# Performance work log

Hardware: AMD Instinct MI355X
Metric: run time of the kernel (lower is better)

The kernel has to match this reference:

```python
import math
import jax, jax.numpy as jnp
import numpy as np

N_FEAT = 4096
EPS = 1e-05
SQRT_LUT = jnp.array([math.isqrt(i * 256 + 128) for i in range(256)], dtype=jnp.int32)


def _ste_round(x):
    # straight-through round: forward round, backward identity
    return x + jax.lax.stop_gradient(jnp.round(x) - x)


def _sqrt_rounded(d):
    # vectorized integer LUT sqrt of d (int32, values in [0, 65535])
    bits = jnp.arange(16, dtype=jnp.int32)
    msb = jnp.sum((d[..., None] >> bits) > 0, axis=-1).astype(jnp.int32) - 1  # bit_length - 1
    k = msb // 2
    norm_shift = (7 - k) * 2
    d_norm = d << norm_shift
    lut_addr = (d_norm >> 8) & 255
    mant = SQRT_LUT[lut_addr]
    q_floor = mant >> (7 - k)
    boundary = q_floor * q_floor + q_floor
    res = jnp.where(d > boundary, q_floor + 1, q_floor)
    return jnp.where(d == 0, 0, res)


def setup_inputs() -> dict:
    key = jax.random.key(0)
    kx, = jax.random.split(key, 1)
    x = jax.random.normal(kx, (8192, N_FEAT), dtype=jnp.float32)
    gamma = jnp.ones((N_FEAT,), dtype=jnp.float32)
    beta = jnp.zeros((N_FEAT,), dtype=jnp.float32)
    return {"x": x, "gamma": gamma, "beta": beta}


def reference(x, gamma, beta):
    # input quantization (per-tensor symmetric int8)
    scale_in = jnp.maximum(jnp.max(jnp.abs(x)) / 127.0, 1e-08)
    x_int = jnp.clip(_ste_round(x / scale_in), -127.0, 127.0)
    x_q = x_int * scale_in
    Ex = jnp.sum(x_q, axis=1, keepdims=True)  # [B,1]
    # LUT-based squaring: split |x_int| into high/low nibbles, x^2 = H^2*256 + 2*H*L*16 + L^2
    X_abs = jnp.abs(x_int).astype(jnp.int32)  # int cast detaches (matches .long())
    H = X_abs >> 4
    L = X_abs & 15
    x_squared_int = (H * H * 256 + H * L * 32 + L * L).astype(jnp.float32)
    x_squared_q = x_squared_int * scale_in ** 2
    Ex2 = jnp.sum(x_squared_q, axis=1, keepdims=True)  # [B,1]
    mu = Ex / N_FEAT
    var = jnp.maximum(Ex2 / N_FEAT - mu * mu, 0.0)
    var_int = jnp.clip(jnp.round(var), 1.0, 2.0 ** 16 - 1).astype(jnp.int32)
    std_int = _sqrt_rounded(var_int).astype(jnp.float32)  # [B,1]
    inv_std = 1.0 / jnp.maximum(std_int, EPS)
    x_norm = (x_q - mu) * inv_std
    y = x_norm * gamma + beta
    # output re-quantization
    scale_out = jnp.maximum(jnp.max(jnp.abs(y)) / 127.0, 1e-08)
    y_int = jnp.clip(_ste_round(y / scale_out), -127.0, 127.0)
    return y_int * scale_out
```

## Files before the change

### kernel.cpp

```cpp
#include <hip/hip_runtime.h>
#include <stdint.h>

#define NFEAT 4096
#define UI_PER_ROW (NFEAT / 4)

#define NSLOT 64
#define SLOT_STRIDE 16

__device__ __forceinline__ int isqrt_floor_small(int v) {
    int m = (int)sqrtf((float)v);
    m -= (m * m > v);
    m += ((m + 1) * (m + 1) <= v);
    return m;
}

__device__ __forceinline__ int sqrt_rounded_ref(int d) {
    if (d <= 0) return 0;
    int msb = 31 - __clz(d);
    int k = msb >> 1;
    int sh = (7 - k) * 2;
    int dn = d << sh;
    int la = (dn >> 8) & 255;
    int mant = isqrt_floor_small(la * 256 + 128);
    int qf = mant >> (7 - k);
    int bnd = qf * qf + qf;
    return (d > bnd) ? (qf + 1) : qf;
}

__device__ __forceinline__ float div_rn(float x, float s, float rs) {
    float q0 = x * rs;
    float r  = fmaf(-s, q0, x);
    return fmaf(r, rs, q0);
}

__device__ __forceinline__ float slot_max(const unsigned* __restrict__ slots) {
    unsigned v = slots[(threadIdx.x & 63) * SLOT_STRIDE];
#pragma unroll
    for (int off = 32; off; off >>= 1) {
        unsigned o = (unsigned)__shfl_xor((int)v, off);
        v = v > o ? v : o;
    }
    return __uint_as_float(v);
}

__global__ __launch_bounds__(256, 4) void absmax_kernel(const float* __restrict__ x,
                                                        int n4,
                                                        unsigned* __restrict__ hx) {
    const float4* x4 = (const float4*)x;
    int i = blockIdx.x * 256 + threadIdx.x;
    const int stride = gridDim.x * 256;
    float m = 0.0f;
    for (; i + 3 * stride < n4; i += 4 * stride) {
        float4 a = x4[i];
        float4 b = x4[i + stride];
        float4 c = x4[i + 2 * stride];
        float4 d = x4[i + 3 * stride];
        float ma = fmaxf(fmaxf(fabsf(a.x), fabsf(a.y)), fmaxf(fabsf(a.z), fabsf(a.w)));
        float mb = fmaxf(fmaxf(fabsf(b.x), fabsf(b.y)), fmaxf(fabsf(b.z), fabsf(b.w)));
        float mc = fmaxf(fmaxf(fabsf(c.x), fabsf(c.y)), fmaxf(fabsf(c.z), fabsf(c.w)));
        float md = fmaxf(fmaxf(fabsf(d.x), fabsf(d.y)), fmaxf(fabsf(d.z), fabsf(d.w)));
        m = fmaxf(m, fmaxf(fmaxf(ma, mb), fmaxf(mc, md)));
    }
    for (; i < n4; i += stride) {
        float4 a = x4[i];
        m = fmaxf(m, fmaxf(fmaxf(fabsf(a.x), fabsf(a.y)), fmaxf(fabsf(a.z), fabsf(a.w))));
    }
#pragma unroll
    for (int off = 32; off; off >>= 1) m = fmaxf(m, __shfl_down(m, off));
    __shared__ float smax[4];
    int lane = threadIdx.x & 63, w = threadIdx.x >> 6;
    if (lane == 0) smax[w] = m;
    __syncthreads();
    if (threadIdx.x == 0) {
        m = fmaxf(fmaxf(smax[0], smax[1]), fmaxf(smax[2], smax[3]));
        atomicMax(hx + (blockIdx.x & (NSLOT - 1)) * SLOT_STRIDE, __float_as_uint(m));
    }
}

template <bool WQ>
__global__ __launch_bounds__(256, 4) void rowstat_kernel(
    const float* __restrict__ x, const float* __restrict__ gamma,
    const float* __restrict__ beta, const unsigned* __restrict__ hx,
    unsigned* __restrict__ hy,
    float* __restrict__ row_mu, float* __restrict__ row_inv,
    uint32_t* __restrict__ xq8) {
#pragma clang fp contract(off)
    const int row = blockIdx.x;
    const int t = threadIdx.x;
    const float4* xr = (const float4*)(x + (size_t)row * NFEAT);
    float4 v0 = xr[t];
    float4 v1 = xr[256 + t];
    float4 v2 = xr[512 + t];
    float4 v3 = xr[768 + t];
    const float s  = fmaxf(slot_max(hx) / 127.0f, 1e-8f);
    const float rs = 1.0f / s;

    float xv[16] = {v0.x, v0.y, v0.z, v0.w, v1.x, v1.y, v1.z, v1.w,
                    v2.x, v2.y, v2.z, v2.w, v3.x, v3.y, v3.z, v3.w};
    int xi[16];
    int s1 = 0, s2 = 0;
#pragma unroll
    for (int k = 0; k < 16; ++k) {
        float q = rintf(div_rn(xv[k], s, rs));
        q = fminf(fmaxf(q, -127.0f), 127.0f);
        int qi = (int)q;
        xi[k] = qi;
        s1 += qi;
        s2 += qi * qi;
    }
    if (WQ) {
        uint32_t* xw = xq8 + (size_t)row * UI_PER_ROW;
#pragma unroll
        for (int g = 0; g < 4; ++g) {
            uint32_t p = (uint32_t)(xi[4 * g + 0] & 255) |
                         ((uint32_t)(xi[4 * g + 1] & 255) << 8) |
                         ((uint32_t)(xi[4 * g + 2] & 255) << 16) |
                         ((uint32_t)xi[4 * g + 3] << 24);
            xw[g * 256 + t] = p;
        }
    }
#pragma unroll
    for (int off = 32; off; off >>= 1) {
        s1 += __shfl_down(s1, off);
        s2 += __shfl_down(s2, off);
    }
    __shared__ int a1[4], a2[4];
    __shared__ float smu, sinv;
    const int lane = t & 63, w = t >> 6;
    if (lane == 0) { a1[w] = s1; a2[w] = s2; }
    __syncthreads();
    if (t == 0) {
        int Exi = a1[0] + a1[1] + a1[2] + a1[3];
        int Ex2i = a2[0] + a2[1] + a2[2] + a2[3];
        float Ex = (float)Exi * s;
        float Ex2 = (float)Ex2i * s * s;
        float mu = Ex / (float)NFEAT;
        float var = fmaxf(Ex2 / (float)NFEAT - mu * mu, 0.0f);
        float vr = fminf(fmaxf(rintf(var), 1.0f), 65535.0f);
        int std_int = sqrt_rounded_ref((int)vr);
        float inv_std = 1.0f / fmaxf((float)std_int, 1e-5f);
        row_mu[row] = mu;
        row_inv[row] = inv_std;
        smu = mu;
        sinv = inv_std;
    }
    __syncthreads();
    const float mu = smu, inv = sinv;
    float ym = 0.0f;
#pragma unroll
    for (int g = 0; g < 4; ++g) {
        float4 gm = ((const float4*)gamma)[g * 256 + t];
        float4 bt = ((const float4*)beta)[g * 256 + t];
        float gv[4] = {gm.x, gm.y, gm.z, gm.w};
        float bv[4] = {bt.x, bt.y, bt.z, bt.w};
#pragma unroll
        for (int j = 0; j < 4; ++j) {
            float xq = (float)xi[g * 4 + j] * s;
            float xn = (xq - mu) * inv;
            float y = xn * gv[j] + bv[j];
            ym = fmaxf(ym, fabsf(y));
        }
    }
#pragma unroll
    for (int off = 32; off; off >>= 1) ym = fmaxf(ym, __shfl_down(ym, off));
    __shared__ float aym[4];
    if (lane == 0) aym[w] = ym;
    __syncthreads();
    if (t == 0) {
        float m = fmaxf(fmaxf(aym[0], aym[1]), fmaxf(aym[2], aym[3]));
        atomicMax(hy + (row & (NSLOT - 1)) * SLOT_STRIDE, __float_as_uint(m));
    }
}

__global__ __launch_bounds__(256, 4) void quantout_q_kernel(
    const uint32_t* __restrict__ xq8, const float* __restrict__ gamma,
    const float* __restrict__ beta, const unsigned* __restrict__ hx,
    const unsigned* __restrict__ hy,
    const float* __restrict__ row_mu, const float* __restrict__ row_inv,
    float* __restrict__ out) {
#pragma clang fp contract(off)
    const int row = blockIdx.x;
    const int t = threadIdx.x;
    const uint32_t* xr = xq8 + (size_t)row * UI_PER_ROW;
    uint32_t p0 = xr[t];
    uint32_t p1 = xr[256 + t];
    uint32_t p2 = xr[512 + t];
    uint32_t p3 = xr[768 + t];
    const float s_in  = fmaxf(slot_max(hx) / 127.0f, 1e-8f);
    const float s_out = fmaxf(slot_max(hy) / 127.0f, 1e-8f);
    const float rso = 1.0f / s_out;
    const float mu = row_mu[row], inv = row_inv[row];
    uint32_t pp[4] = {p0, p1, p2, p3};
    float4* outr = (float4*)(out + (size_t)row * NFEAT);
#pragma unroll
    for (int g = 0; g < 4; ++g) {
        uint32_t p = pp[g];
        float4 gm = ((const float4*)gamma)[g * 256 + t];
        float4 bt = ((const float4*)beta)[g * 256 + t];
        float gv[4] = {gm.x, gm.y, gm.z, gm.w};
        float bv[4] = {bt.x, bt.y, bt.z, bt.w};
        int xs[4] = {(int)(int8_t)(p & 255), (int)(int8_t)((p >> 8) & 255),
                     (int)(int8_t)((p >> 16) & 255), (int)(int8_t)((p >> 24) & 255)};
        float o[4];
#pragma unroll
        for (int j = 0; j < 4; ++j) {
            float xq = (float)xs[j] * s_in;
            float xn = (xq - mu) * inv;
            float y = xn * gv[j] + bv[j];
            float q = rintf(div_rn(y, s_out, rso));
            q = fminf(fmaxf(q, -127.0f), 127.0f);
            o[j] = q * s_out;
        }
        outr[g * 256 + t] = make_float4(o[0], o[1], o[2], o[3]);
    }
}

__global__ __launch_bounds__(256, 4) void quantout_f_kernel(
    const float* __restrict__ x, const float* __restrict__ gamma,
    const float* __restrict__ beta, const unsigned* __restrict__ hx,
    const unsigned* __restrict__ hy,
    const float* __restrict__ row_mu, const float* __restrict__ row_inv,
    float* __restrict__ out) {
#pragma clang fp contract(off)
    const int row = blockIdx.x;
    const int t = threadIdx.x;
    const float4* xr = (const float4*)(x + (size_t)row * NFEAT);
    float4 w0 = xr[t];
    float4 w1 = xr[256 + t];
    float4 w2 = xr[512 + t];
    float4 w3 = xr[768 + t];
    const float s_in  = fmaxf(slot_max(hx) / 127.0f, 1e-8f);
    const float s_out = fmaxf(slot_max(hy) / 127.0f, 1e-8f);
    const float rsi = 1.0f / s_in;
    const float rso = 1.0f / s_out;
    const float mu = row_mu[row], inv = row_inv[row];
    float4 vv[4] = {w0, w1, w2, w3};
    float4* outr = (float4*)(out + (size_t)row * NFEAT);
#pragma unroll
    for (int g = 0; g < 4; ++g) {
        float4 v = vv[g];
        float4 gm = ((const float4*)gamma)[g * 256 + t];
        float4 bt = ((const float4*)beta)[g * 256 + t];
        float xv[4] = {v.x, v.y, v.z, v.w};
        float gv[4] = {gm.x, gm.y, gm.z, gm.w};
        float bv[4] = {bt.x, bt.y, bt.z, bt.w};
        float o[4];
#pragma unroll
        for (int j = 0; j < 4; ++j) {
            float q = rintf(div_rn(xv[j], s_in, rsi));
            q = fminf(fmaxf(q, -127.0f), 127.0f);
            float xq = q * s_in;
            float xn = (xq - mu) * inv;
            float y = xn * gv[j] + bv[j];
            float qq = rintf(div_rn(y, s_out, rso));
            qq = fminf(fmaxf(qq, -127.0f), 127.0f);
            o[j] = qq * s_out;
        }
        outr[g * 256 + t] = make_float4(o[0], o[1], o[2], o[3]);
    }
}

extern "C" void kernel_launch(void* const* d_in, const int* in_sizes, int n_in,
                              void* d_out, int out_size, void* d_ws, size_t ws_size,
                              hipStream_t stream) {
    const float* x = (const float*)d_in[0];
    const float* gamma = (const float*)d_in[1];
    const float* beta = (const float*)d_in[2];
    float* out = (float*)d_out;

    const int total = in_sizes[0];
    const int rows = total / NFEAT;

    char* ws = (char*)d_ws;
    unsigned* hx = (unsigned*)ws;
    unsigned* hy = (unsigned*)(ws + 4096);
    float* row_mu = (float*)(ws + 8192);
    float* row_inv = row_mu + rows;
    size_t xq_off = (8192 + (size_t)rows * 8 + 255) & ~(size_t)255;
    uint32_t* xq8 = (uint32_t*)(ws + xq_off);
    const bool use_q = ws_size >= xq_off + (size_t)total + 256;

    hipMemsetAsync(ws, 0, 8192, stream);

    absmax_kernel<<<2048, 256, 0, stream>>>(x, total / 4, hx);

    if (use_q) {
        rowstat_kernel<true><<<rows, 256, 0, stream>>>(x, gamma, beta, hx, hy,
                                                       row_mu, row_inv, xq8);
        quantout_q_kernel<<<rows, 256, 0, stream>>>(xq8, gamma, beta, hx, hy,
                                                    row_mu, row_inv, out);
    } else {
        rowstat_kernel<false><<<rows, 256, 0, stream>>>(x, gamma, beta, hx, hy,
                                                        row_mu, row_inv, nullptr);
        quantout_f_kernel<<<rows, 256, 0, stream>>>(x, gamma, beta, hx, hy,
                                                    row_mu, row_inv, out);
    }
}
```

Measured before the change: 275.3 us.

## Fuse absmax, row stats and requantization into one cooperative grid-synced kernel

Replaces the memset plus three separate launches with a single cooperative kernel of 256 blocks of 1024 threads. Each block owns 32 rows and uses grid-wide syncs between the global absmax, the row-statistics/output-absmax pass and the final requantization pass. Per-block partial maxima go to plain slots instead of atomics, and the int8 staging buffer is dropped, so x is re-read from global memory in the last pass. This removes launch gaps and the memset, but adds grid-sync cost, relies on cooperative launch co-residency, and reads x three times (128 MB each), which may partly hit in cache.

```diff
diff --git a/kernel.cpp b/kernel.cpp
--- a/kernel.cpp
+++ b/kernel.cpp
@@ -1,8 +1,14 @@
 #include <hip/hip_runtime.h>
+#include <hip/hip_cooperative_groups.h>
 #include <stdint.h>
+
+namespace cg = cooperative_groups;
 
 #define NFEAT 4096
 #define UI_PER_ROW (NFEAT / 4)
+#define GRID 256
+#define BLK 1024
+#define ROWS_PB 32
 
 #define NSLOT 64
 #define SLOT_STRIDE 16
@@ -33,7 +39,182 @@
     return fmaf(r, rs, q0);
 }
 
-__device__ __forceinline__ float slot_max(const unsigned* __restrict__ slots) {
+__device__ __forceinline__ float slots256_max(const unsigned* __restrict__ s, int lane) {
+    unsigned v = s[lane];
+    unsigned a = s[lane + 64], b = s[lane + 128], c = s[lane + 192];
+    v = v > a ? v : a;
+    v = v > b ? v : b;
+    v = v > c ? v : c;
+#pragma unroll
+    for (int off = 32; off; off >>= 1) {
+        unsigned o = (unsigned)__shfl_xor((int)v, off);
+        v = v > o ? v : o;
+    }
+    return __uint_as_float(v);
+}
+
+__global__ __launch_bounds__(BLK, 4) void fused_kernel(
+    const float* __restrict__ x, const float* __restrict__ gamma,
+    const float* __restrict__ beta, float* __restrict__ out,
+    unsigned* __restrict__ slot, unsigned* __restrict__ slot2, int rows) {
+#pragma clang fp contract(off)
+    cg::grid_group gridg = cg::this_grid();
+    const int bid = blockIdx.x;
+    const int t = threadIdx.x;
+    const int lane = t & 63;
+    const int wave = t >> 6;
+
+    __shared__ int a1s[16], a2s[16];
+    __shared__ float redf[16];
+    __shared__ float smu[ROWS_PB], sinv[ROWS_PB];
+
+    {
+        const float4* x4 = (const float4*)x;
+        const int n4 = rows * (NFEAT / 4);
+        const int stride = GRID * BLK;
+        int i = bid * BLK + t;
+        float m = 0.0f;
+        for (; i + 3 * stride < n4; i += 4 * stride) {
+            float4 a = x4[i];
+            float4 b = x4[i + stride];
+            float4 c = x4[i + 2 * stride];
+            float4 d = x4[i + 3 * stride];
+            float ma = fmaxf(fmaxf(fabsf(a.x), fabsf(a.y)), fmaxf(fabsf(a.z), fabsf(a.w)));
+            float mb = fmaxf(fmaxf(fabsf(b.x), fabsf(b.y)), fmaxf(fabsf(b.z), fabsf(b.w)));
+            float mc = fmaxf(fmaxf(fabsf(c.x), fabsf(c.y)), fmaxf(fabsf(c.z), fabsf(c.w)));
+            float md = fmaxf(fmaxf(fabsf(d.x), fabsf(d.y)), fmaxf(fabsf(d.z), fabsf(d.w)));
+            m = fmaxf(m, fmaxf(fmaxf(ma, mb), fmaxf(mc, md)));
+        }
+        for (; i < n4; i += stride) {
+            float4 a = x4[i];
+            m = fmaxf(m, fmaxf(fmaxf(fabsf(a.x), fabsf(a.y)), fmaxf(fabsf(a.z), fabsf(a.w))));
+        }
+#pragma unroll
+        for (int off = 32; off; off >>= 1) m = fmaxf(m, __shfl_down(m, off));
+        if (lane == 0) redf[wave] = m;
+        __syncthreads();
+        if (t == 0) {
+            float mm = redf[0];
+#pragma unroll
+            for (int i2 = 1; i2 < 16; ++i2) mm = fmaxf(mm, redf[i2]);
+            slot[bid] = __float_as_uint(mm);
+        }
+    }
+    gridg.sync();
+
+    const float s  = fmaxf(slots256_max(slot, lane) / 127.0f, 1e-8f);
+    const float rs = 1.0f / s;
+    const int rb = t >> 8;
+    const int tr = t & 255;
+    const int nb = ROWS_PB / 4;
+    float ym = 0.0f;
+    for (int b = 0; b < nb; ++b) {
+        const int r = bid * ROWS_PB + b * 4 + rb;
+        const float4* xr = (const float4*)(x + (size_t)r * NFEAT);
+        float4 v0 = xr[tr];
+        float4 v1 = xr[256 + tr];
+        float4 v2 = xr[512 + tr];
+        float4 v3 = xr[768 + tr];
+        float xv[16] = {v0.x, v0.y, v0.z, v0.w, v1.x, v1.y, v1.z, v1.w,
+                        v2.x, v2.y, v2.z, v2.w, v3.x, v3.y, v3.z, v3.w};
+        int xi[16];
+        int s1 = 0, s2 = 0;
+#pragma unroll
+        for (int k = 0; k < 16; ++k) {
+            float q = rintf(div_rn(xv[k], s, rs));
+            q = fminf(fmaxf(q, -127.0f), 127.0f);
+            int qi = (int)q;
+            xi[k] = qi;
+            s1 += qi;
+            s2 += qi * qi;
+        }
+#pragma unroll
+        for (int off = 32; off; off >>= 1) {
+            s1 += __shfl_down(s1, off);
+            s2 += __shfl_down(s2, off);
+        }
+        if (lane == 0) { a1s[wave] = s1; a2s[wave] = s2; }
+        __syncthreads();
+        if (tr == 0) {
+            const int w0 = rb * 4;
+            int Exi  = a1s[w0] + a1s[w0 + 1] + a1s[w0 + 2] + a1s[w0 + 3];
+            int Ex2i = a2s[w0] + a2s[w0 + 1] + a2s[w0 + 2] + a2s[w0 + 3];
+            float Ex  = (float)Exi * s;
+            float Ex2 = (float)Ex2i * s * s;
+            float mu  = Ex / (float)NFEAT;
+            float var = fmaxf(Ex2 / (float)NFEAT - mu * mu, 0.0f);
+            float vr  = fminf(fmaxf(rintf(var), 1.0f), 65535.0f);
+            int std_int = sqrt_rounded_ref((int)vr);
+            float inv = 1.0f / fmaxf((float)std_int, 1e-5f);
+            smu[b * 4 + rb]  = mu;
+            sinv[b * 4 + rb] = inv;
+        }
+        __syncthreads();
+        const float mu = smu[b * 4 + rb], inv = sinv[b * 4 + rb];
+#pragma unroll
+        for (int g = 0; g < 4; ++g) {
+            float4 gm = ((const float4*)gamma)[g * 256 + tr];
+            float4 bt = ((const float4*)beta)[g * 256 + tr];
+            float gv[4] = {gm.x, gm.y, gm.z, gm.w};
+            float bv[4] = {bt.x, bt.y, bt.z, bt.w};
+#pragma unroll
+            for (int j = 0; j < 4; ++j) {
+                float xq = (float)xi[g * 4 + j] * s;
+                float xn = (xq - mu) * inv;
+                float y = xn * gv[j] + bv[j];
+                ym = fmaxf(ym, fabsf(y));
+            }
+        }
+    }
+#pragma unroll
+    for (int off = 32; off; off >>= 1) ym = fmaxf(ym, __shfl_down(ym, off));
+    if (lane == 0) redf[wave] = ym;
+    __syncthreads();
+    if (t == 0) {
+        float mm = redf[0];
+#pragma unroll
+        for (int i2 = 1; i2 < 16; ++i2) mm = fmaxf(mm, redf[i2]);
+        slot2[bid] = __float_as_uint(mm);
+    }
+    gridg.sync();
+
+    const float so  = fmaxf(slots256_max(slot2, lane) / 127.0f, 1e-8f);
+    const float rso = 1.0f / so;
+    for (int b = 0; b < nb; ++b) {
+        const int r = bid * ROWS_PB + b * 4 + rb;
+        const float4* xr = (const float4*)(x + (size_t)r * NFEAT);
+        float4 v0 = xr[tr];
+        float4 v1 = xr[256 + tr];
+        float4 v2 = xr[512 + tr];
+        float4 v3 = xr[768 + tr];
+        float xv[16] = {v0.x, v0.y, v0.z, v0.w, v1.x, v1.y, v1.z, v1.w,
+                        v2.x, v2.y, v2.z, v2.w, v3.x, v3.y, v3.z, v3.w};
+        const float mu = smu[b * 4 + rb], inv = sinv[b * 4 + rb];
+        float4* outr = (float4*)(out + (size_t)r * NFEAT);
+#pragma unroll
+        for (int g = 0; g < 4; ++g) {
+            float4 gm = ((const float4*)gamma)[g * 256 + tr];
+            float4 bt = ((const float4*)beta)[g * 256 + tr];
+            float gv[4] = {gm.x, gm.y, gm.z, gm.w};
+            float bv[4] = {bt.x, bt.y, bt.z, bt.w};
+            float o[4];
+#pragma unroll
+            for (int j = 0; j < 4; ++j) {
+                float q = rintf(div_rn(xv[g * 4 + j], s, rs));
+                q = fminf(fmaxf(q, -127.0f), 127.0f);
+                float xq = q * s;
+                float xn = (xq - mu) * inv;
+                float y = xn * gv[j] + bv[j];
+                float qq = rintf(div_rn(y, so, rso));
+                qq = fminf(fmaxf(qq, -127.0f), 127.0f);
+                o[j] = qq * so;
+            }
+            outr[g * 256 + tr] = make_float4(o[0], o[1], o[2], o[3]);
+        }
+    }
+}
+
+__device__ __forceinline__ float slot_max64(const unsigned* __restrict__ slots) {
     unsigned v = slots[(threadIdx.x & 63) * SLOT_STRIDE];
 #pragma unroll
     for (int off = 32; off; off >>= 1) {
@@ -77,13 +258,11 @@
     }
 }
 
-template <bool WQ>
 __global__ __launch_bounds__(256, 4) void rowstat_kernel(
     const float* __restrict__ x, const float* __restrict__ gamma,
     const float* __restrict__ beta, const unsigned* __restrict__ hx,
     unsigned* __restrict__ hy,
-    float* __restrict__ row_mu, float* __restrict__ row_inv,
-    uint32_t* __restrict__ xq8) {
+    float* __restrict__ row_mu, float* __restrict__ row_inv) {
 #pragma clang fp contract(off)
     const int row = blockIdx.x;
     const int t = threadIdx.x;
@@ -92,7 +271,7 @@
     float4 v1 = xr[256 + t];
     float4 v2 = xr[512 + t];
     float4 v3 = xr[768 + t];
-    const float s  = fmaxf(slot_max(hx) / 127.0f, 1e-8f);
+    const float s  = fmaxf(slot_max64(hx) / 127.0f, 1e-8f);
     const float rs = 1.0f / s;
 
     float xv[16] = {v0.x, v0.y, v0.z, v0.w, v1.x, v1.y, v1.z, v1.w,
@@ -108,24 +287,13 @@
         s1 += qi;
         s2 += qi * qi;
     }
-    if (WQ) {
-        uint32_t* xw = xq8 + (size_t)row * UI_PER_ROW;
-#pragma unroll
-        for (int g = 0; g < 4; ++g) {
-            uint32_t p = (uint32_t)(xi[4 * g + 0] & 255) |
-                         ((uint32_t)(xi[4 * g + 1] & 255) << 8) |
-                         ((uint32_t)(xi[4 * g + 2] & 255) << 16) |
-                         ((uint32_t)xi[4 * g + 3] << 24);
-            xw[g * 256 + t] = p;
-        }
-    }
 #pragma unroll
     for (int off = 32; off; off >>= 1) {
         s1 += __shfl_down(s1, off);
         s2 += __shfl_down(s2, off);
     }
     __shared__ int a1[4], a2[4];
-    __shared__ float smu, sinv;
+    __shared__ float smu1, sinv1;
     const int lane = t & 63, w = t >> 6;
     if (lane == 0) { a1[w] = s1; a2[w] = s2; }
     __syncthreads();
@@ -141,11 +309,11 @@
         float inv_std = 1.0f / fmaxf((float)std_int, 1e-5f);
         row_mu[row] = mu;
         row_inv[row] = inv_std;
-        smu = mu;
-        sinv = inv_std;
+        smu1 = mu;
+        sinv1 = inv_std;
     }
     __syncthreads();
-    const float mu = smu, inv = sinv;
+    const float mu = smu1, inv = sinv1;
     float ym = 0.0f;
 #pragma unroll
     for (int g = 0; g < 4; ++g) {
@@ -169,49 +337,6 @@
     if (t == 0) {
         float m = fmaxf(fmaxf(aym[0], aym[1]), fmaxf(aym[2], aym[3]));
         atomicMax(hy + (row & (NSLOT - 1)) * SLOT_STRIDE, __float_as_uint(m));
-    }
-}
-
-__global__ __launch_bounds__(256, 4) void quantout_q_kernel(
-    const uint32_t* __restrict__ xq8, const float* __restrict__ gamma,
-    const float* __restrict__ beta, const unsigned* __restrict__ hx,
-    const unsigned* __restrict__ hy,
-    const float* __restrict__ row_mu, const float* __restrict__ row_inv,
-    float* __restrict__ out) {
-#pragma clang fp contract(off)
-    const int row = blockIdx.x;
-    const int t = threadIdx.x;
-    const uint32_t* xr = xq8 + (size_t)row * UI_PER_ROW;
-    uint32_t p0 = xr[t];
-    uint32_t p1 = xr[256 + t];
-    uint32_t p2 = xr[512 + t];
-    uint32_t p3 = xr[768 + t];
-    const float s_in  = fmaxf(slot_max(hx) / 127.0f, 1e-8f);
-    const float s_out = fmaxf(slot_max(hy) / 127.0f, 1e-8f);
-    const float rso = 1.0f / s_out;
-    const float mu = row_mu[row], inv = row_inv[row];
-    uint32_t pp[4] = {p0, p1, p2, p3};
-    float4* outr = (float4*)(out + (size_t)row * NFEAT);
-#pragma unroll
-    for (int g = 0; g < 4; ++g) {
-        uint32_t p = pp[g];
-        float4 gm = ((const float4*)gamma)[g * 256 + t];
-        float4 bt = ((const float4*)beta)[g * 256 + t];
-        float gv[4] = {gm.x, gm.y, gm.z, gm.w};
-        float bv[4] = {bt.x, bt.y, bt.z, bt.w};
-        int xs[4] = {(int)(int8_t)(p & 255), (int)(int8_t)((p >> 8) & 255),
-                     (int)(int8_t)((p >> 16) & 255), (int)(int8_t)((p >> 24) & 255)};
-        float o[4];
-#pragma unroll
-        for (int j = 0; j < 4; ++j) {
-            float xq = (float)xs[j] * s_in;
-            float xn = (xq - mu) * inv;
-            float y = xn * gv[j] + bv[j];
-            float q = rintf(div_rn(y, s_out, rso));
-            q = fminf(fmaxf(q, -127.0f), 127.0f);
-            o[j] = q * s_out;
-        }
-        outr[g * 256 + t] = make_float4(o[0], o[1], o[2], o[3]);
     }
 }
 
@@ -229,8 +354,8 @@
     float4 w1 = xr[256 + t];
     float4 w2 = xr[512 + t];
     float4 w3 = xr[768 + t];
-    const float s_in  = fmaxf(slot_max(hx) / 127.0f, 1e-8f);
-    const float s_out = fmaxf(slot_max(hy) / 127.0f, 1e-8f);
+    const float s_in  = fmaxf(slot_max64(hx) / 127.0f, 1e-8f);
+    const float s_out = fmaxf(slot_max64(hy) / 127.0f, 1e-8f);
     const float rsi = 1.0f / s_in;
     const float rso = 1.0f / s_out;
     const float mu = row_mu[row], inv = row_inv[row];
@@ -269,30 +394,30 @@
     float* out = (float*)d_out;
 
     const int total = in_sizes[0];
-    const int rows = total / NFEAT;
+    int rows = total / NFEAT;
 
     char* ws = (char*)d_ws;
+    unsigned* slot  = (unsigned*)ws;
+    unsigned* slot2 = (unsigned*)(ws + 2048);
+
+    if (rows == GRID * ROWS_PB) {
+        void* args[] = {(void*)&x, (void*)&gamma, (void*)&beta, (void*)&out,
+                        (void*)&slot, (void*)&slot2, (void*)&rows};
+        hipError_t e = hipLaunchCooperativeKernel((void*)fused_kernel,
+                                                  dim3(GRID), dim3(BLK),
+                                                  args, 0, stream);
+        if (e == hipSuccess) return;
+    }
+
     unsigned* hx = (unsigned*)ws;
     unsigned* hy = (unsigned*)(ws + 4096);
     float* row_mu = (float*)(ws + 8192);
     float* row_inv = row_mu + rows;
-    size_t xq_off = (8192 + (size_t)rows * 8 + 255) & ~(size_t)255;
-    uint32_t* xq8 = (uint32_t*)(ws + xq_off);
-    const bool use_q = ws_size >= xq_off + (size_t)total + 256;
 
     hipMemsetAsync(ws, 0, 8192, stream);
-
     absmax_kernel<<<2048, 256, 0, stream>>>(x, total / 4, hx);
-
-    if (use_q) {
-        rowstat_kernel<true><<<rows, 256, 0, stream>>>(x, gamma, beta, hx, hy,
-                                                       row_mu, row_inv, xq8);
-        quantout_q_kernel<<<rows, 256, 0, stream>>>(xq8, gamma, beta, hx, hy,
-                                                    row_mu, row_inv, out);
-    } else {
-        rowstat_kernel<false><<<rows, 256, 0, stream>>>(x, gamma, beta, hx, hy,
-                                                        row_mu, row_inv, nullptr);
-        quantout_f_kernel<<<rows, 256, 0, stream>>>(x, gamma, beta, hx, hy,
-                                                    row_mu, row_inv, out);
-    }
-}
+    rowstat_kernel<<<rows, 256, 0, stream>>>(x, gamma, beta, hx, hy,
+                                             row_mu, row_inv);
+    quantout_f_kernel<<<rows, 256, 0, stream>>>(x, gamma, beta, hx, hy,
+                                                row_mu, row_inv, out);
+}
```

After: 342.5 us. 1.24x slower.

## Replace atomic max slots with per-block partials and one-row-per-wave row stats

Applied to the files above, without the earlier changes.

The global absmax reductions now write one partial per block instead of doing atomicMax into 64 slots, which removes the memset launch and atomic contention. Consumers read and reduce up to 2048 partials per block in wave 0. Row statistics now run with one wave per row, using shuffle-only reductions and no block-level barrier for mu and variance. This adds redundant partial-reading work in every consumer block and may lower per-row memory parallelism.

```diff
diff --git a/kernel.cpp b/kernel.cpp
--- a/kernel.cpp
+++ b/kernel.cpp
@@ -2,10 +2,7 @@
 #include <stdint.h>
 
 #define NFEAT 4096
-#define UI_PER_ROW (NFEAT / 4)
-
-#define NSLOT 64
-#define SLOT_STRIDE 16
+#define ABS_GRID 2048
 
 __device__ __forceinline__ int isqrt_floor_small(int v) {
     int m = (int)sqrtf((float)v);
@@ -33,22 +30,27 @@
     return fmaf(r, rs, q0);
 }
 
-__device__ __forceinline__ float slot_max(const unsigned* __restrict__ slots) {
-    unsigned v = slots[(threadIdx.x & 63) * SLOT_STRIDE];
+__device__ __forceinline__ unsigned slots_max_u(const unsigned* __restrict__ s,
+                                                int n, int lane) {
+    unsigned v = 0;
+    for (int i = lane; i < n; i += 64) {
+        unsigned a = s[i];
+        v = v > a ? v : a;
+    }
 #pragma unroll
     for (int off = 32; off; off >>= 1) {
         unsigned o = (unsigned)__shfl_xor((int)v, off);
         v = v > o ? v : o;
     }
-    return __uint_as_float(v);
-}
-
-__global__ __launch_bounds__(256, 4) void absmax_kernel(const float* __restrict__ x,
-                                                        int n4,
-                                                        unsigned* __restrict__ hx) {
+    return v;
+}
+
+__global__ __launch_bounds__(256, 4) void absmax_ps(const float* __restrict__ x,
+                                                    int n4,
+                                                    unsigned* __restrict__ hx) {
     const float4* x4 = (const float4*)x;
     int i = blockIdx.x * 256 + threadIdx.x;
-    const int stride = gridDim.x * 256;
+    const int stride = ABS_GRID * 256;
     float m = 0.0f;
     for (; i + 3 * stride < n4; i += 4 * stride) {
         float4 a = x4[i];
@@ -73,28 +75,184 @@
     __syncthreads();
     if (threadIdx.x == 0) {
         m = fmaxf(fmaxf(smax[0], smax[1]), fmaxf(smax[2], smax[3]));
-        atomicMax(hx + (blockIdx.x & (NSLOT - 1)) * SLOT_STRIDE, __float_as_uint(m));
-    }
-}
-
-template <bool WQ>
-__global__ __launch_bounds__(256, 4) void rowstat_kernel(
+        hx[blockIdx.x] = __float_as_uint(m);
+    }
+}
+
+__global__ __launch_bounds__(256, 4) void rowstat_wave(
     const float* __restrict__ x, const float* __restrict__ gamma,
     const float* __restrict__ beta, const unsigned* __restrict__ hx,
     unsigned* __restrict__ hy,
     float* __restrict__ row_mu, float* __restrict__ row_inv,
     uint32_t* __restrict__ xq8) {
 #pragma clang fp contract(off)
+    const int bid = blockIdx.x;
+    const int t = threadIdx.x;
+    const int lane = t & 63;
+    const int wave = t >> 6;
+    const float4* g4 = (const float4*)gamma;
+    const float4* b4 = (const float4*)beta;
+
+    __shared__ float sS;
+    __shared__ float redf[4];
+
+    if (wave == 0) {
+        unsigned mb = slots_max_u(hx, ABS_GRID, lane);
+        if (lane == 0) sS = fmaxf(__uint_as_float(mb) / 127.0f, 1e-8f);
+    }
+    __syncthreads();
+    const float s  = sS;
+    const float rs = 1.0f / s;
+
+    const int row = bid * 4 + wave;
+    const float4* xr = (const float4*)(x + (size_t)row * NFEAT);
+
+    uint32_t pk[16];
+    int s1 = 0, s2 = 0;
+#pragma unroll 4
+    for (int c = 0; c < 16; ++c) {
+        float4 v = xr[c * 64 + lane];
+        float q0 = rintf(div_rn(v.x, s, rs));
+        float q1 = rintf(div_rn(v.y, s, rs));
+        float q2 = rintf(div_rn(v.z, s, rs));
+        float q3 = rintf(div_rn(v.w, s, rs));
+        q0 = fminf(fmaxf(q0, -127.0f), 127.0f);
+        q1 = fminf(fmaxf(q1, -127.0f), 127.0f);
+        q2 = fminf(fmaxf(q2, -127.0f), 127.0f);
+        q3 = fminf(fmaxf(q3, -127.0f), 127.0f);
+        int i0 = (int)q0, i1 = (int)q1, i2 = (int)q2, i3 = (int)q3;
+        pk[c] = (uint32_t)(i0 & 255) | ((uint32_t)(i1 & 255) << 8) |
+                ((uint32_t)(i2 & 255) << 16) | ((uint32_t)i3 << 24);
+        s1 += i0 + i1 + i2 + i3;
+        s2 += i0 * i0 + i1 * i1 + i2 * i2 + i3 * i3;
+    }
+#pragma unroll
+    for (int off = 32; off; off >>= 1) {
+        s1 += __shfl_xor(s1, off);
+        s2 += __shfl_xor(s2, off);
+    }
+    float Ex  = (float)s1 * s;
+    float Ex2 = (float)s2 * s * s;
+    float mu  = Ex / (float)NFEAT;
+    float var = fmaxf(Ex2 / (float)NFEAT - mu * mu, 0.0f);
+    float vr  = fminf(fmaxf(rintf(var), 1.0f), 65535.0f);
+    int sdi   = sqrt_rounded_ref((int)vr);
+    float inv = 1.0f / fmaxf((float)sdi, 1e-5f);
+    if (lane == 0) {
+        row_mu[row]  = mu;
+        row_inv[row] = inv;
+    }
+
+    uint32_t* xw = xq8 + (size_t)row * (NFEAT / 4);
+#pragma unroll 4
+    for (int c = 0; c < 16; ++c) xw[c * 64 + lane] = pk[c];
+
+    float ym = 0.0f;
+#pragma unroll 4
+    for (int c = 0; c < 16; ++c) {
+        uint32_t p = pk[c];
+        float4 gm = g4[c * 64 + lane];
+        float4 bt = b4[c * 64 + lane];
+        int i0 = (int)(int8_t)(p & 255);
+        int i1 = (int)(int8_t)((p >> 8) & 255);
+        int i2 = (int)(int8_t)((p >> 16) & 255);
+        int i3 = (int)(int8_t)((p >> 24) & 255);
+        float y0 = ((float)i0 * s - mu) * inv * gm.x + bt.x;
+        float y1 = ((float)i1 * s - mu) * inv * gm.y + bt.y;
+        float y2 = ((float)i2 * s - mu) * inv * gm.z + bt.z;
+        float y3 = ((float)i3 * s - mu) * inv * gm.w + bt.w;
+        ym = fmaxf(ym, fmaxf(fmaxf(fabsf(y0), fabsf(y1)),
+                             fmaxf(fabsf(y2), fabsf(y3))));
+    }
+#pragma unroll
+    for (int off = 32; off; off >>= 1) ym = fmaxf(ym, __shfl_down(ym, off));
+    if (lane == 0) redf[wave] = ym;
+    __syncthreads();
+    if (t == 0) {
+        hy[bid] = __float_as_uint(fmaxf(fmaxf(redf[0], redf[1]),
+                                        fmaxf(redf[2], redf[3])));
+    }
+}
+
+__global__ __launch_bounds__(256, 4) void quantout_q2(
+    const uint32_t* __restrict__ xq8, const float* __restrict__ gamma,
+    const float* __restrict__ beta, const unsigned* __restrict__ hx,
+    const unsigned* __restrict__ hy, int n_hy,
+    const float* __restrict__ row_mu, const float* __restrict__ row_inv,
+    float* __restrict__ out) {
+#pragma clang fp contract(off)
     const int row = blockIdx.x;
     const int t = threadIdx.x;
+    const int lane = t & 63;
+    const int wave = t >> 6;
+
+    __shared__ float sIn, sOut;
+    if (wave == 0) {
+        unsigned a = slots_max_u(hx, ABS_GRID, lane);
+        unsigned b = slots_max_u(hy, n_hy, lane);
+        if (lane == 0) {
+            sIn  = fmaxf(__uint_as_float(a) / 127.0f, 1e-8f);
+            sOut = fmaxf(__uint_as_float(b) / 127.0f, 1e-8f);
+        }
+    }
+    __syncthreads();
+    const float s_in  = sIn;
+    const float s_out = sOut;
+    const float rso = 1.0f / s_out;
+    const float mu = row_mu[row], inv = row_inv[row];
+
+    const uint32_t* xr = xq8 + (size_t)row * (NFEAT / 4);
+    uint32_t p0 = xr[t];
+    uint32_t p1 = xr[256 + t];
+    uint32_t p2 = xr[512 + t];
+    uint32_t p3 = xr[768 + t];
+    uint32_t pp[4] = {p0, p1, p2, p3};
+    float4* outr = (float4*)(out + (size_t)row * NFEAT);
+#pragma unroll
+    for (int g = 0; g < 4; ++g) {
+        uint32_t p = pp[g];
+        float4 gm = ((const float4*)gamma)[g * 256 + t];
+        float4 bt = ((const float4*)beta)[g * 256 + t];
+        float gv[4] = {gm.x, gm.y, gm.z, gm.w};
+        float bv[4] = {bt.x, bt.y, bt.z, bt.w};
+        int xs[4] = {(int)(int8_t)(p & 255), (int)(int8_t)((p >> 8) & 255),
+                     (int)(int8_t)((p >> 16) & 255), (int)(int8_t)((p >> 24) & 255)};
+        float o[4];
+#pragma unroll
+        for (int j = 0; j < 4; ++j) {
+            float xq = (float)xs[j] * s_in;
+            float xn = (xq - mu) * inv;
+            float y = xn * gv[j] + bv[j];
+            float q = rintf(div_rn(y, s_out, rso));
+            q = fminf(fmaxf(q, -127.0f), 127.0f);
+            o[j] = q * s_out;
+        }
+        outr[g * 256 + t] = make_float4(o[0], o[1], o[2], o[3]);
+    }
+}
+
+__global__ __launch_bounds__(256, 4) void rowstat_blk(
+    const float* __restrict__ x, const float* __restrict__ gamma,
+    const float* __restrict__ beta, const unsigned* __restrict__ hx,
+    unsigned* __restrict__ hy,
+    float* __restrict__ row_mu, float* __restrict__ row_inv) {
+#pragma clang fp contract(off)
+    const int row = blockIdx.x;
+    const int t = threadIdx.x;
+    const int lane = t & 63, w = t >> 6;
+    __shared__ float sS;
+    if (w == 0) {
+        unsigned mb = slots_max_u(hx, ABS_GRID, lane);
+        if (lane == 0) sS = fmaxf(__uint_as_float(mb) / 127.0f, 1e-8f);
+    }
+    __syncthreads();
+    const float s = sS;
+    const float rs = 1.0f / s;
     const float4* xr = (const float4*)(x + (size_t)row * NFEAT);
     float4 v0 = xr[t];
     float4 v1 = xr[256 + t];
     float4 v2 = xr[512 + t];
     float4 v3 = xr[768 + t];
-    const float s  = fmaxf(slot_max(hx) / 127.0f, 1e-8f);
-    const float rs = 1.0f / s;
-
     float xv[16] = {v0.x, v0.y, v0.z, v0.w, v1.x, v1.y, v1.z, v1.w,
                     v2.x, v2.y, v2.z, v2.w, v3.x, v3.y, v3.z, v3.w};
     int xi[16];
@@ -108,25 +266,13 @@
         s1 += qi;
         s2 += qi * qi;
     }
-    if (WQ) {
-        uint32_t* xw = xq8 + (size_t)row * UI_PER_ROW;
-#pragma unroll
-        for (int g = 0; g < 4; ++g) {
-            uint32_t p = (uint32_t)(xi[4 * g + 0] & 255) |
-                         ((uint32_t)(xi[4 * g + 1] & 255) << 8) |
-                         ((uint32_t)(xi[4 * g + 2] & 255) << 16) |
-                         ((uint32_t)xi[4 * g + 3] << 24);
-            xw[g * 256 + t] = p;
-        }
-    }
 #pragma unroll
     for (int off = 32; off; off >>= 1) {
         s1 += __shfl_down(s1, off);
         s2 += __shfl_down(s2, off);
     }
     __shared__ int a1[4], a2[4];
-    __shared__ float smu, sinv;
-    const int lane = t & 63, w = t >> 6;
+    __shared__ float smu1, sinv1;
     if (lane == 0) { a1[w] = s1; a2[w] = s2; }
     __syncthreads();
     if (t == 0) {
@@ -141,11 +287,11 @@
         float inv_std = 1.0f / fmaxf((float)std_int, 1e-5f);
         row_mu[row] = mu;
         row_inv[row] = inv_std;
-        smu = mu;
-        sinv = inv_std;
-    }
-    __syncthreads();
-    const float mu = smu, inv = sinv;
+        smu1 = mu;
+        sinv1 = inv_std;
+    }
+    __syncthreads();
+    const float mu = smu1, inv = sinv1;
     float ym = 0.0f;
 #pragma unroll
     for (int g = 0; g < 4; ++g) {
@@ -166,79 +312,40 @@
     __shared__ float aym[4];
     if (lane == 0) aym[w] = ym;
     __syncthreads();
-    if (t == 0) {
-        float m = fmaxf(fmaxf(aym[0], aym[1]), fmaxf(aym[2], aym[3]));
-        atomicMax(hy + (row & (NSLOT - 1)) * SLOT_STRIDE, __float_as_uint(m));
-    }
-}
-
-__global__ __launch_bounds__(256, 4) void quantout_q_kernel(
-    const uint32_t* __restrict__ xq8, const float* __restrict__ gamma,
+    if (t == 0)
+        hy[row] = __float_as_uint(fmaxf(fmaxf(aym[0], aym[1]),
+                                        fmaxf(aym[2], aym[3])));
+}
+
+__global__ __launch_bounds__(256, 4) void quantout_f2(
+    const float* __restrict__ x, const float* __restrict__ gamma,
     const float* __restrict__ beta, const unsigned* __restrict__ hx,
-    const unsigned* __restrict__ hy,
+    const unsigned* __restrict__ hy, int n_hy,
     const float* __restrict__ row_mu, const float* __restrict__ row_inv,
     float* __restrict__ out) {
 #pragma clang fp contract(off)
     const int row = blockIdx.x;
     const int t = threadIdx.x;
-    const uint32_t* xr = xq8 + (size_t)row * UI_PER_ROW;
-    uint32_t p0 = xr[t];
-    uint32_t p1 = xr[256 + t];
-    uint32_t p2 = xr[512 + t];
-    uint32_t p3 = xr[768 + t];
-    const float s_in  = fmaxf(slot_max(hx) / 127.0f, 1e-8f);
-    const float s_out = fmaxf(slot_max(hy) / 127.0f, 1e-8f);
-    const float rso = 1.0f / s_out;
-    const float mu = row_mu[row], inv = row_inv[row];
-    uint32_t pp[4] = {p0, p1, p2, p3};
-    float4* outr = (float4*)(out + (size_t)row * NFEAT);
-#pragma unroll
-    for (int g = 0; g < 4; ++g) {
-        uint32_t p = pp[g];
-        float4 gm = ((const float4*)gamma)[g * 256 + t];
-        float4 bt = ((const float4*)beta)[g * 256 + t];
-        float gv[4] = {gm.x, gm.y, gm.z, gm.w};
-        float bv[4] = {bt.x, bt.y, bt.z, bt.w};
-        int xs[4] = {(int)(int8_t)(p & 255), (int)(int8_t)((p >> 8) & 255),
-                     (int)(int8_t)((p >> 16) & 255), (int)(int8_t)((p >> 24) & 255)};
-        float o[4];
-#pragma unroll
-        for (int j = 0; j < 4; ++j) {
-            float xq = (float)xs[j] * s_in;
-            float xn = (xq - mu) * inv;
-            float y = xn * gv[j] + bv[j];
-            float q = rintf(div_rn(y, s_out, rso));
-            q = fminf(fmaxf(q, -127.0f), 127.0f);
-            o[j] = q * s_out;
+    const int lane = t & 63, w = t >> 6;
+    __shared__ float sIn, sOut;
+    if (w == 0) {
+        unsigned a = slots_max_u(hx, ABS_GRID, lane);
+        unsigned b = slots_max_u(hy, n_hy, lane);
+        if (lane == 0) {
+            sIn  = fmaxf(__uint_as_float(a) / 127.0f, 1e-8f);
+            sOut = fmaxf(__uint_as_float(b) / 127.0f, 1e-8f);
         }
-        outr[g * 256 + t] = make_float4(o[0], o[1], o[2], o[3]);
-    }
-}
-
-__global__ __launch_bounds__(256, 4) void quantout_f_kernel(
-    const float* __restrict__ x, const float* __restrict__ gamma,
-    const float* __restrict__ beta, const unsigned* __restrict__ hx,
-    const unsigned* __restrict__ hy,
-    const float* __restrict__ row_mu, const float* __restrict__ row_inv,
-    float* __restrict__ out) {
-#pragma clang fp contract(off)
-    const int row = blockIdx.x;
-    const int t = threadIdx.x;
-    const float4* xr = (const float4*)(x + (size_t)row * NFEAT);
-    float4 w0 = xr[t];
-    float4 w1 = xr[256 + t];
-    float4 w2 = xr[512 + t];
-    float4 w3 = xr[768 + t];
-    const float s_in  = fmaxf(slot_max(hx) / 127.0f, 1e-8f);
-    const float s_out = fmaxf(slot_max(hy) / 127.0f, 1e-8f);
+    }
+    __syncthreads();
+    const float s_in = sIn, s_out = sOut;
     const float rsi = 1.0f / s_in;
     const float rso = 1.0f / s_out;
     const float mu = row_mu[row], inv = row_inv[row];
-    float4 vv[4] = {w0, w1, w2, w3};
+    const float4* xr = (const float4*)(x + (size_t)row * NFEAT);
     float4* outr = (float4*)(out + (size_t)row * NFEAT);
 #pragma unroll
     for (int g = 0; g < 4; ++g) {
-        float4 v = vv[g];
+        float4 v = xr[g * 256 + t];
         float4 gm = ((const float4*)gamma)[g * 256 + t];
         float4 bt = ((const float4*)beta)[g * 256 + t];
         float xv[4] = {v.x, v.y, v.z, v.w};
@@ -273,26 +380,26 @@
 
     char* ws = (char*)d_ws;
     unsigned* hx = (unsigned*)ws;
-    unsigned* hy = (unsigned*)(ws + 4096);
-    float* row_mu = (float*)(ws + 8192);
+    unsigned* hy = (unsigned*)(ws + 8192);
+    float* row_mu = (float*)(ws + 65536);
     float* row_inv = row_mu + rows;
-    size_t xq_off = (8192 + (size_t)rows * 8 + 255) & ~(size_t)255;
+    size_t xq_off = (65536 + (size_t)rows * 8 + 255) & ~(size_t)255;
     uint32_t* xq8 = (uint32_t*)(ws + xq_off);
-    const bool use_q = ws_size >= xq_off + (size_t)total + 256;
-
-    hipMemsetAsync(ws, 0, 8192, stream);
-
-    absmax_kernel<<<2048, 256, 0, stream>>>(x, total / 4, hx);
-
-    if (use_q) {
-        rowstat_kernel<true><<<rows, 256, 0, stream>>>(x, gamma, beta, hx, hy,
-                                                       row_mu, row_inv, xq8);
-        quantout_q_kernel<<<rows, 256, 0, stream>>>(xq8, gamma, beta, hx, hy,
-                                                    row_mu, row_inv, out);
+    const bool fast = (rows % 4 == 0) && rows >= 4 &&
+                      ws_size >= xq_off + (size_t)total + 256 &&
+                      (size_t)rows * 4 + 8192 <= 65536;
+
+    absmax_ps<<<ABS_GRID, 256, 0, stream>>>(x, total / 4, hx);
+
+    if (fast) {
+        rowstat_wave<<<rows / 4, 256, 0, stream>>>(x, gamma, beta, hx, hy,
+                                                   row_mu, row_inv, xq8);
+        quantout_q2<<<rows, 256, 0, stream>>>(xq8, gamma, beta, hx, hy,
+                                              rows / 4, row_mu, row_inv, out);
     } else {
-        rowstat_kernel<false><<<rows, 256, 0, stream>>>(x, gamma, beta, hx, hy,
-                                                        row_mu, row_inv, nullptr);
-        quantout_f_kernel<<<rows, 256, 0, stream>>>(x, gamma, beta, hx, hy,
-                                                    row_mu, row_inv, out);
-    }
-}
+        rowstat_blk<<<rows, 256, 0, stream>>>(x, gamma, beta, hx, hy,
+                                              row_mu, row_inv);
+        quantout_f2<<<rows, 256, 0, stream>>>(x, gamma, beta, hx, hy,
+                                              rows, row_mu, row_inv, out);
+    }
+}
```

Result: slower. 295.3 us (+7.3%).
